# Kernel tuning notes

Hardware: AMD Instinct MI355X
Metric: run time of the kernel (lower is better)

## Reference

```python
import jax, jax.numpy as jnp
import numpy as np

D_MODEL = 1024
NUM_HEADS = 16
HEAD_DIM = D_MODEL // NUM_HEADS  # 64
SCALE = HEAD_DIM ** -0.5
BIAS_LEN = 128  # min(max_seq_len=512, 128)
ROPE_BASE = 10000.0
LN_EPS = 1e-5


def setup_inputs() -> dict:
    key = jax.random.key(0)
    ks = jax.random.split(key, 8)
    B, Lq, Lkv = 8, 512, 512
    return {
        "decoder_hidden": jax.random.normal(ks[0], (B, Lq, D_MODEL), jnp.float32),
        "encoder_output": jax.random.normal(ks[1], (B, Lkv, D_MODEL), jnp.float32),
        "Wqkv": jax.random.normal(ks[2], (3 * D_MODEL, D_MODEL), jnp.float32) * 0.02,
        "Wout": jax.random.normal(ks[3], (D_MODEL, D_MODEL), jnp.float32) * 0.02,
        "b_out": jnp.zeros((D_MODEL,), jnp.float32),
        "Wgate": jax.random.normal(ks[4], (D_MODEL, D_MODEL), jnp.float32) * 0.02,
        "b_gate": jnp.zeros((D_MODEL,), jnp.float32),
        "gamma": jnp.ones((D_MODEL,), jnp.float32),
        "beta": jnp.zeros((D_MODEL,), jnp.float32),
    }


def _layernorm(x, gamma, beta):
    mu = jnp.mean(x, axis=-1, keepdims=True)
    var = jnp.mean(jnp.square(x - mu), axis=-1, keepdims=True)
    return (x - mu) * jax.lax.rsqrt(var + LN_EPS) * gamma + beta


def _rope(x, cos, sin):
    # x: [B, H, L, HEAD_DIM]; cos/sin: [L, HEAD_DIM//2]
    half = HEAD_DIM // 2
    c = cos[None, None, :, :]
    s = sin[None, None, :, :]
    x_even, x_odd = x[..., :half], x[..., half:]
    return jnp.concatenate([x_even * c - x_odd * s, x_even * s + x_odd * c], axis=-1)


def _temporal_bias(L_q, L_kv):
    pos = jnp.arange(BIAS_LEN, dtype=jnp.float32)
    dist = jnp.abs(pos[None, :] - pos[:, None])  # [128,128]
    bias = jnp.exp(-dist * 0.1) - dist * 0.05
    if L_q <= BIAS_LEN and L_kv <= BIAS_LEN:
        return bias[:L_q, :L_kv]
    # bilinear interpolation (align_corners=False / half-pixel) fallback
    return jax.image.resize(bias, (L_q, L_kv), method="bilinear")


def reference(decoder_hidden, encoder_output, Wqkv, Wout, b_out, Wgate, b_gate, gamma, beta):
    B, L_q, _ = decoder_hidden.shape
    L_kv = encoder_output.shape[1]
    residual = decoder_hidden

    q_in = _layernorm(decoder_hidden, gamma, beta)
    kv_in = _layernorm(encoder_output, gamma, beta)

    q = q_in @ Wqkv[:D_MODEL].T
    k = kv_in @ Wqkv[D_MODEL:2 * D_MODEL].T
    v = kv_in @ Wqkv[2 * D_MODEL:].T

    q = q.reshape(B, L_q, NUM_HEADS, HEAD_DIM).transpose(0, 2, 1, 3)
    k = k.reshape(B, L_kv, NUM_HEADS, HEAD_DIM).transpose(0, 2, 1, 3)
    v = v.reshape(B, L_kv, NUM_HEADS, HEAD_DIM).transpose(0, 2, 1, 3)

    # rotary embedding over max(L_q, L_kv) positions
    L = max(L_q, L_kv)
    inv_freq = 1.0 / ROPE_BASE ** (jnp.arange(0, HEAD_DIM, 2, dtype=jnp.float32) / HEAD_DIM)
    freqs = jnp.arange(L, dtype=jnp.float32)[:, None] * inv_freq[None, :]  # [L, HEAD_DIM//2]
    cos, sin = jnp.cos(freqs), jnp.sin(freqs)
    q = _rope(q, cos[:L_q], sin[:L_q])
    k = _rope(k, cos[:L_kv], sin[:L_kv])

    scores = jnp.einsum("bhqd,bhkd->bhqk", q, k) * SCALE
    scores = scores + _temporal_bias(L_q, L_kv)[None, None, :, :]

    attn = jax.nn.softmax(scores, axis=-1)
    attended = jnp.einsum("bhqk,bhkd->bhqd", attn, v)
    attended = attended.transpose(0, 2, 1, 3).reshape(B, L_q, D_MODEL)
    attended = attended @ Wout.T + b_out

    gate = jax.nn.sigmoid(attended @ Wgate.T + b_gate)
    output = gate * attended + (1.0 - gate) * residual
    return output
```

## Files before the change

kernel.cpp:

```cpp
#include <hip/hip_runtime.h>
#include <hip/hip_bf16.h>

#define D_MODEL 1024
#define NHEADS 16
#define HDIM 64
#define BATCH 8
#define SEQ 512
#define NROWS 4096
#define SCALE 0.125f
#define LN_EPS 1e-5f

typedef __attribute__((ext_vector_type(8))) short bf16x8;
typedef __attribute__((ext_vector_type(4))) float f32x4;
typedef __attribute__((ext_vector_type(8))) unsigned short u16x8;

static __device__ __forceinline__ float bf2f(unsigned short u) {
    return __uint_as_float(((unsigned int)u) << 16);
}
static __device__ __forceinline__ unsigned short f2bf(float f) {
    unsigned int x = __float_as_uint(f);
    unsigned int r = (x + 0x7fffu + ((x >> 16) & 1u)) >> 16;
    return (unsigned short)r;
}

#define GLOAD16(gp, lp)                                                        \
    __builtin_amdgcn_global_load_lds(                                          \
        (const __attribute__((address_space(1))) void*)(gp),                   \
        (__attribute__((address_space(3))) void*)(lp), 16, 0, 0)

static __device__ __forceinline__ float bias128(int a, int b) {
    float d = fabsf((float)(a - b));
    return expf(-d * 0.1f) - d * 0.05f;
}

__global__ void prep_kernel(const float* __restrict__ dec, const float* __restrict__ enc,
                            const float* __restrict__ gamma, const float* __restrict__ beta,
                            const float* __restrict__ Wqkv,
                            const float* __restrict__ Wout, const float* __restrict__ Wgate,
                            unsigned short* __restrict__ q_ln, unsigned short* __restrict__ kv_ln,
                            float* __restrict__ bias, unsigned short* __restrict__ Wqkv_bf,
                            unsigned short* __restrict__ Wout_bf, unsigned short* __restrict__ Wgate_bf) {
    int blk = blockIdx.x;
    int t = threadIdx.x;
    if (blk >= 12288) {
        int idx = (blk - 12288) * 256 + t;
        const float* src; unsigned short* dst; int off;
        if (idx < 262144) { src = Wout; dst = Wout_bf; off = idx; }
        else              { src = Wgate; dst = Wgate_bf; off = idx - 262144; }
        float4 v = ((const float4*)src)[off];
        ushort4 u;
        u.x = f2bf(v.x); u.y = f2bf(v.y); u.z = f2bf(v.z); u.w = f2bf(v.w);
        ((ushort4*)dst)[off] = u;
        return;
    }
    if (blk >= 9216) {
        int idx = (blk - 9216) * 256 + t;
        float4 v = ((const float4*)Wqkv)[idx];
        ushort4 u;
        u.x = f2bf(v.x); u.y = f2bf(v.y); u.z = f2bf(v.z); u.w = f2bf(v.w);
        ((ushort4*)Wqkv_bf)[idx] = u;
        return;
    }
    if (blk >= 8192) {
        int idx = (blk - 8192) * 256 + t;
        int qi = idx >> 9, kj = idx & 511;
        float fq = (qi + 0.5f) * 0.25f - 0.5f;
        float fk = (kj + 0.5f) * 0.25f - 0.5f;
        int iq = (int)floorf(fq); float tq = fq - (float)iq;
        int ik = (int)floorf(fk); float tk = fk - (float)ik;
        int iq0 = min(max(iq, 0), 127), iq1 = min(max(iq + 1, 0), 127);
        int ik0 = min(max(ik, 0), 127), ik1 = min(max(ik + 1, 0), 127);
        float v = (1.f - tq) * ((1.f - tk) * bias128(iq0, ik0) + tk * bias128(iq0, ik1))
                +        tq  * ((1.f - tk) * bias128(iq1, ik0) + tk * bias128(iq1, ik1));
        bias[idx] = v;
        return;
    }
    int row = blk;
    const float* src = (row < NROWS) ? dec + (size_t)row * D_MODEL
                                     : enc + (size_t)(row - NROWS) * D_MODEL;
    unsigned short* dst = (row < NROWS) ? q_ln + (size_t)row * D_MODEL
                                        : kv_ln + (size_t)(row - NROWS) * D_MODEL;
    float4 x = ((const float4*)src)[t];
    float s  = x.x + x.y + x.z + x.w;
    float ss = x.x * x.x + x.y * x.y + x.z * x.z + x.w * x.w;
    #pragma unroll
    for (int off = 32; off > 0; off >>= 1) {
        s  += __shfl_down(s, off);
        ss += __shfl_down(ss, off);
    }
    __shared__ float red_s[4], red_ss[4];
    int wid = t >> 6, lane = t & 63;
    if (lane == 0) { red_s[wid] = s; red_ss[wid] = ss; }
    __syncthreads();
    if (t == 0) {
        float S = red_s[0] + red_s[1] + red_s[2] + red_s[3];
        float SS = red_ss[0] + red_ss[1] + red_ss[2] + red_ss[3];
        red_s[0] = S; red_ss[0] = SS;
    }
    __syncthreads();
    float mu  = red_s[0] * (1.0f / 1024.0f);
    float var = red_ss[0] * (1.0f / 1024.0f) - mu * mu;
    float rstd = rsqrtf(var + LN_EPS);
    float4 g = ((const float4*)gamma)[t];
    float4 bb = ((const float4*)beta)[t];
    ushort4 u;
    u.x = f2bf((x.x - mu) * rstd * g.x + bb.x);
    u.y = f2bf((x.y - mu) * rstd * g.y + bb.y);
    u.z = f2bf((x.z - mu) * rstd * g.z + bb.z);
    u.w = f2bf((x.w - mu) * rstd * g.w + bb.w);
    ((ushort4*)dst)[t] = u;
}

__global__ void convert_og(const float* __restrict__ Wout, const float* __restrict__ Wgate,
                           unsigned short* __restrict__ Wout_bf, unsigned short* __restrict__ Wgate_bf) {
    int idx = blockIdx.x * 256 + threadIdx.x;
    const float* src; unsigned short* dst; int off;
    if (idx < 262144) { src = (const float*)Wout; dst = Wout_bf; off = idx; }
    else              { src = (const float*)Wgate; dst = Wgate_bf; off = idx - 262144; }
    float4 v = ((const float4*)src)[off];
    ushort4 u;
    u.x = f2bf(v.x); u.y = f2bf(v.y); u.z = f2bf(v.z); u.w = f2bf(v.w);
    ((ushort4*)dst)[off] = u;
}

#define CSTR 136

struct alignas(16) Smem64B {
    unsigned short A[64 * 128];
    unsigned short B[128 * 128];
};

#define MF(a, b, d) __builtin_amdgcn_mfma_f32_16x16x32_bf16((a), (b), (d), 0, 0, 0)

#define GEMM_KH2B(kh)                                                          \
    {                                                                          \
        int pofs = (((kh) * 4 + quad) ^ c) * 8;                                \
        const unsigned short* Arow_ = &As2[(wr * 32 + c) * 128 + pofs];        \
        const unsigned short* Brow_ = &Bs2[(wc * 64 + c) * 128 + pofs];        \
        bf16x8 f0 = *(const bf16x8*)(Arow_);                                   \
        bf16x8 f1 = *(const bf16x8*)(Arow_ + 2048);                            \
        bf16x8 g0 = *(const bf16x8*)(Brow_);                                   \
        bf16x8 g1 = *(const bf16x8*)(Brow_ + 2048);                            \
        bf16x8 g2 = *(const bf16x8*)(Brow_ + 4096);                            \
        bf16x8 g3 = *(const bf16x8*)(Brow_ + 6144);                            \
        c00 = MF(f0, g0, c00); c01 = MF(f0, g1, c01); c02 = MF(f0, g2, c02); c03 = MF(f0, g3, c03); \
        c10 = MF(f1, g0, c10); c11 = MF(f1, g1, c11); c12 = MF(f1, g2, c12); c13 = MF(f1, g3, c13); \
    }

#define GEMM_BODY_64B(Aptr, Bptr)                                              \
    int wave = tid >> 6, lane = tid & 63, quad = lane >> 4, c = lane & 15;     \
    int wr = wave >> 1, wc = wave & 1;                                         \
    int l4 = lane >> 4, l15 = lane & 15;                                       \
    const unsigned short* Abase = (Aptr) + (size_t)(rt * 64) * 1024;           \
    const unsigned short* Bbase = (Bptr) + (size_t)(ct * 128) * 1024;          \
    int aoff0 = (wave * 16 +  0 + l4) * 1024 + ((l15 ^ ( 0 + l4)) * 8);        \
    int aoff1 = (wave * 16 +  4 + l4) * 1024 + ((l15 ^ ( 4 + l4)) * 8);        \
    int aoff2 = (wave * 16 +  8 + l4) * 1024 + ((l15 ^ ( 8 + l4)) * 8);        \
    int aoff3 = (wave * 16 + 12 + l4) * 1024 + ((l15 ^ (12 + l4)) * 8);        \
    int boff0 = (wave * 32 +  0 + l4) * 1024 + ((l15 ^ (( 0 + l4) & 15)) * 8); \
    int boff1 = (wave * 32 +  4 + l4) * 1024 + ((l15 ^ (( 4 + l4) & 15)) * 8); \
    int boff2 = (wave * 32 +  8 + l4) * 1024 + ((l15 ^ (( 8 + l4) & 15)) * 8); \
    int boff3 = (wave * 32 + 12 + l4) * 1024 + ((l15 ^ ((12 + l4) & 15)) * 8); \
    int boff4 = (wave * 32 + 16 + l4) * 1024 + ((l15 ^ ((16 + l4) & 15)) * 8); \
    int boff5 = (wave * 32 + 20 + l4) * 1024 + ((l15 ^ ((20 + l4) & 15)) * 8); \
    int boff6 = (wave * 32 + 24 + l4) * 1024 + ((l15 ^ ((24 + l4) & 15)) * 8); \
    int boff7 = (wave * 32 + 28 + l4) * 1024 + ((l15 ^ ((28 + l4) & 15)) * 8); \
    unsigned short* AsW = As2 + wave * 2048;                                   \
    unsigned short* BsW = Bs2 + wave * 4096;                                   \
    f32x4 c00 = (f32x4)0.f, c01 = (f32x4)0.f, c02 = (f32x4)0.f, c03 = (f32x4)0.f; \
    f32x4 c10 = (f32x4)0.f, c11 = (f32x4)0.f, c12 = (f32x4)0.f, c13 = (f32x4)0.f; \
    for (int kt = 0; kt < 8; ++kt) {                                           \
        int k0 = kt * 128;                                                     \
        __syncthreads();                                                       \
        GLOAD16(Abase + aoff0 + k0, AsW);                                      \
        GLOAD16(Abase + aoff1 + k0, AsW + 512);                                \
        GLOAD16(Abase + aoff2 + k0, AsW + 1024);                               \
        GLOAD16(Abase + aoff3 + k0, AsW + 1536);                               \
        GLOAD16(Bbase + boff0 + k0, BsW);                                      \
        GLOAD16(Bbase + boff1 + k0, BsW + 512);                                \
        GLOAD16(Bbase + boff2 + k0, BsW + 1024);                               \
        GLOAD16(Bbase + boff3 + k0, BsW + 1536);                               \
        GLOAD16(Bbase + boff4 + k0, BsW + 2048);                               \
        GLOAD16(Bbase + boff5 + k0, BsW + 2560);                               \
        GLOAD16(Bbase + boff6 + k0, BsW + 3072);                               \
        GLOAD16(Bbase + boff7 + k0, BsW + 3584);                               \
        __syncthreads();                                                       \
        GEMM_KH2B(0)                                                           \
        GEMM_KH2B(1)                                                           \
        GEMM_KH2B(2)                                                           \
        GEMM_KH2B(3)                                                           \
    }

union alignas(16) SmemQD {
    struct { unsigned short A[2][64 * 64]; unsigned short B[2][128 * 64]; } ab;
    unsigned short C[64 * CSTR];
    unsigned short Ct[128 * 72];
};

#define QSTAGE(pA, pB, k0)                                                     \
    GLOAD16(Ab + (k0),          (pA) + stW);                                   \
    GLOAD16(Ab + 32768 + (k0),  (pA) + stW + 2048);                            \
    GLOAD16(Bb + (k0),          (pB) + stW);                                   \
    GLOAD16(Bb + 32768 + (k0),  (pB) + stW + 2048);                            \
    GLOAD16(Bb + 65536 + (k0),  (pB) + stW + 4096);                            \
    GLOAD16(Bb + 98304 + (k0),  (pB) + stW + 6144);

#define QKH(pA, pB, kh)                                                        \
    {                                                                          \
        int pofs = (((kh) * 4 + quad) ^ x7) * 8;                               \
        const unsigned short* Ar_ = (pA) + (wr * 32 + c) * 64 + pofs;          \
        const unsigned short* Br_ = (pB) + (wc * 64 + c) * 64 + pofs;          \
        bf16x8 f0 = *(const bf16x8*)(Ar_);                                     \
        bf16x8 f1 = *(const bf16x8*)(Ar_ + 1024);                              \
        bf16x8 g0 = *(const bf16x8*)(Br_);                                     \
        bf16x8 g1 = *(const bf16x8*)(Br_ + 1024);                              \
        bf16x8 g2 = *(const bf16x8*)(Br_ + 2048);                              \
        bf16x8 g3 = *(const bf16x8*)(Br_ + 3072);                              \
        c00 = MF(f0, g0, c00); c01 = MF(f0, g1, c01); c02 = MF(f0, g2, c02); c03 = MF(f0, g3, c03); \
        c10 = MF(f1, g0, c10); c11 = MF(f1, g1, c11); c12 = MF(f1, g2, c12); c13 = MF(f1, g3, c13); \
    }

#define QROPE_REG(i, reg, A0, A1, A2, A3)                                      \
    {                                                                          \
        int mloc = wr * 32 + (i) * 16 + quad * 4 + (reg);                      \
        int crow = mloc * CSTR + wc * 64;                                      \
        float fl = (float)((rt * 64 + mloc) & 511);                            \
        float aa0 = fl * inv0, aa1 = fl * inv1;                                \
        float c0 = cosf(aa0), s0 = sinf(aa0);                                  \
        float c1 = cosf(aa1), s1 = sinf(aa1);                                  \
        float e0 = A0[(reg)], o0 = A2[(reg)];                                  \
        float e1 = A1[(reg)], o1 = A3[(reg)];                                  \
        smemq.C[crow + c]      = f2bf(e0 * c0 - o0 * s0);                      \
        smemq.C[crow + 32 + c] = f2bf(e0 * s0 + o0 * c0);                      \
        smemq.C[crow + 16 + c] = f2bf(e1 * c1 - o1 * s1);                      \
        smemq.C[crow + 48 + c] = f2bf(e1 * s1 + o1 * c1);                      \
    }
#define QROPE_ROW(i, A0, A1, A2, A3)                                           \
    QROPE_REG(i, 0, A0, A1, A2, A3) QROPE_REG(i, 1, A0, A1, A2, A3)            \
    QROPE_REG(i, 2, A0, A1, A2, A3) QROPE_REG(i, 3, A0, A1, A2, A3)

#define QVSECT_REG(i, j, reg, Acc)                                             \
    smemq.Ct[(wc * 64 + (j) * 16 + c) * 72 + (wr * 32 + (i) * 16 + quad * 4 + (reg))] = f2bf(Acc[(reg)]);
#define QVSECT_TILE(i, j, Acc)                                                 \
    QVSECT_REG(i, j, 0, Acc) QVSECT_REG(i, j, 1, Acc)                          \
    QVSECT_REG(i, j, 2, Acc) QVSECT_REG(i, j, 3, Acc)

__global__ __launch_bounds__(256, 1)
void qkv_gemm_mfma(const unsigned short* __restrict__ q_ln,
                   const unsigned short* __restrict__ kv_ln,
                   const unsigned short* __restrict__ Wb,
                   unsigned short* __restrict__ qo,
                   unsigned short* __restrict__ ko,
                   unsigned short* __restrict__ vo) {
    int bid = blockIdx.x;
    int wg = (bid & 7) * 192 + (bid >> 3);
    int st = wg >> 5, in = wg & 31;
    int stc = st >> 4, str = st & 15;
    int ct = stc * 8 + (in & 7);
    int rt = str * 4 + (in >> 3);
    int n0 = ct * 128;
    int section = stc;
    const unsigned short* A = (section == 0) ? q_ln : kv_ln;

    __shared__ SmemQD smemq;
    int tid = threadIdx.x;
    int wave = tid >> 6, lane = tid & 63, quad = lane >> 4, c = lane & 15;
    int wr = wave >> 1, wc = wave & 1;
    int x7 = c & 7;

    int soff = (tid >> 3) * 1024 + (((tid & 7) ^ ((tid >> 3) & 7)) * 8);
    const unsigned short* Ab = A + (size_t)(rt * 64) * 1024 + soff;
    const unsigned short* Bb = Wb + (size_t)n0 * 1024 + soff;
    int stW = wave * 512;
    unsigned short* A0 = smemq.ab.A[0];
    unsigned short* A1 = smemq.ab.A[1];
    unsigned short* B0 = smemq.ab.B[0];
    unsigned short* B1 = smemq.ab.B[1];

    f32x4 c00 = (f32x4)0.f, c01 = (f32x4)0.f, c02 = (f32x4)0.f, c03 = (f32x4)0.f;
    f32x4 c10 = (f32x4)0.f, c11 = (f32x4)0.f, c12 = (f32x4)0.f, c13 = (f32x4)0.f;

    QSTAGE(A0, B0, 0)
    __syncthreads();
    for (int kt2 = 0; kt2 < 8; ++kt2) {
        QSTAGE(A1, B1, (kt2 * 2 + 1) * 64)
        QKH(A0, B0, 0) QKH(A0, B0, 1)
        __syncthreads();
        if (kt2 < 7) { QSTAGE(A0, B0, (kt2 * 2 + 2) * 64) }
        QKH(A1, B1, 0) QKH(A1, B1, 1)
        __syncthreads();
    }

    if (section == 2) {
        QVSECT_TILE(0, 0, c00) QVSECT_TILE(0, 1, c01) QVSECT_TILE(0, 2, c02) QVSECT_TILE(0, 3, c03)
        QVSECT_TILE(1, 0, c10) QVSECT_TILE(1, 1, c11) QVSECT_TILE(1, 2, c12) QVSECT_TILE(1, 3, c13)
        __syncthreads();
        int dr = tid >> 1, hh = tid & 1;
        int h = ((n0 & 1023) >> 6) + (dr >> 6);
        int d = dr & 63;
        int mmb = rt * 64;
        int bb = mmb >> 9, ll0 = mmb & 511;
        unsigned short* orow = vo + (((size_t)bb * NHEADS + h) * HDIM + d) * SEQ + ll0 + hh * 32;
        const unsigned short* csrc = &smemq.Ct[dr * 72 + hh * 32];
        #pragma unroll
        for (int kc = 0; kc < 4; ++kc)
            *(u16x8*)(orow + kc * 8) = *(const u16x8*)(csrc + kc * 8);
        return;
    }

    float inv0 = expf(-0.2878231366f * (float)c);
    float inv1 = expf(-0.2878231366f * (float)(16 + c));
    QROPE_ROW(0, c00, c01, c02, c03)
    QROPE_ROW(1, c10, c11, c12, c13)
    __syncthreads();

    unsigned short* outp = (section == 0) ? qo : ko;
    int rr = tid >> 2;
    int ch = (tid >> 1) & 1;
    int sub = tid & 1;
    int mm = rt * 64 + rr;
    int bb = mm >> 9, ll = mm & 511;
    int h = ((n0 & 1023) >> 6) + ch;
    unsigned short* orow = outp + (((size_t)bb * NHEADS + h) * SEQ + ll) * HDIM + sub * 32;
    const unsigned short* csrc = &smemq.C[rr * CSTR + ch * 64 + sub * 32];
    #pragma unroll
    for (int kc = 0; kc < 4; ++kc)
        *(u16x8*)(orow + kc * 8) = *(const u16x8*)(csrc + kc * 8);
}

#define O1_REG(mb, reg, n, Acc)                                                \
    t_bf[(size_t)((mb) + (reg)) * 1024 + (n)] = f2bf(Acc[(reg)] + bo);
#define O1_TILE(i, j, Acc)                                                     \
    {                                                                          \
        int n = ct * 128 + wc * 64 + (j) * 16 + c;                             \
        float bo = b_out[n];                                                   \
        int mb = rt * 64 + wr * 32 + (i) * 16 + quad * 4;                      \
        O1_REG(mb, 0, n, Acc) O1_REG(mb, 1, n, Acc)                            \
        O1_REG(mb, 2, n, Acc) O1_REG(mb, 3, n, Acc)                            \
    }

__global__ __launch_bounds__(256, 1)
void out_gemm1_mfma(const unsigned short* __restrict__ att,
                    const unsigned short* __restrict__ Wob,
                    const float* __restrict__ b_out,
                    unsigned short* __restrict__ t_bf) {
    int ct = blockIdx.x, rt = blockIdx.y;
    __shared__ Smem64B smem2;
    unsigned short* As2 = smem2.A;
    unsigned short* Bs2 = smem2.B;
    int tid = threadIdx.x;

    GEMM_BODY_64B(att, Wob)

    O1_TILE(0, 0, c00) O1_TILE(0, 1, c01) O1_TILE(0, 2, c02) O1_TILE(0, 3, c03)
    O1_TILE(1, 0, c10) O1_TILE(1, 1, c11) O1_TILE(1, 2, c12) O1_TILE(1, 3, c13)
}

#define O2_REG(mb, reg, n, Acc)                                                \
    {                                                                          \
        float gz = Acc[(reg)] + bg;                                            \
        float g = 1.0f / (1.0f + expf(-gz));                                   \
        size_t idx = (size_t)((mb) + (reg)) * 1024 + (n);                      \
        float tv = bf2f(t_bf[idx]);                                            \
        float rv = residual[idx];                                              \
        out[idx] = g * tv + (1.0f - g) * rv;                                   \
    }
#define O2_TILE(i, j, Acc)                                                     \
    {                                                                          \
        int n = ct * 128 + wc * 64 + (j) * 16 + c;                             \
        float bg = b_gate[n];                                                  \
        int mb = rt * 64 + wr * 32 + (i) * 16 + quad * 4;                      \
        O2_REG(mb, 0, n, Acc) O2_REG(mb, 1, n, Acc)                            \
        O2_REG(mb, 2, n, Acc) O2_REG(mb, 3, n, Acc)                            \
    }

__global__ __launch_bounds__(256, 1)
void out_gemm2_mfma(const unsigned short* __restrict__ t_bf,
                    const unsigned short* __restrict__ Wgb,
                    const float* __restrict__ b_gate,
                    const float* __restrict__ residual,
                    float* __restrict__ out) {
    int ct = blockIdx.x, rt = blockIdx.y;
    __shared__ Smem64B smem2;
    unsigned short* As2 = smem2.A;
    unsigned short* Bs2 = smem2.B;
    int tid = threadIdx.x;

    GEMM_BODY_64B(t_bf, Wgb)

    O2_TILE(0, 0, c00) O2_TILE(0, 1, c01) O2_TILE(0, 2, c02) O2_TILE(0, 3, c03)
    O2_TILE(1, 0, c10) O2_TILE(1, 1, c11) O2_TILE(1, 2, c12) O2_TILE(1, 3, c13)
}

#define KSTR 72

__global__ __launch_bounds__(512)
void attn_kernel(const unsigned short* __restrict__ q,
                 const unsigned short* __restrict__ k,
                 const unsigned short* __restrict__ vt,
                 const float* __restrict__ bias,
                 unsigned short* __restrict__ attended) {
    int qt = blockIdx.x, h = blockIdx.y, b = blockIdx.z;
    __shared__ unsigned short Ks[64 * 64];
    __shared__ unsigned short Vs[64 * 64];
    __shared__ unsigned short Ps[128 * KSTR];
    __shared__ float lf[128];

    int tid = threadIdx.x;
    int wave = tid >> 6, lane = tid & 63;
    int quad = lane >> 4, c = lane & 15;
    int wb = wave * 16;
    size_t headbase = (((size_t)b * NHEADS + h) * SEQ) * HDIM;
    int q0 = qt * 128;

    const unsigned short* qrow = q + headbase + (size_t)(q0 + wb + c) * HDIM;
    bf16x8 aq0 = *(const bf16x8*)(qrow + quad * 8);
    bf16x8 aq1 = *(const bf16x8*)(qrow + 32 + quad * 8);

    int srow = wave * 8 + (lane >> 3);
    int schunk = (lane & 7) ^ (srow & 7);
    unsigned short* KsW = Ks + wave * 512;
    unsigned short* VsW = Vs + wave * 512;
    const unsigned short* kgb = k + headbase + (size_t)srow * HDIM + schunk * 8;
    const unsigned short* vgb = vt + headbase + (size_t)srow * SEQ + schunk * 8;
    int x7 = c & 7;
    int p0 = (quad ^ x7) * 8;
    int p1 = ((4 + quad) ^ x7) * 8;

    f32x4 oacc[4];
    #pragma unroll
    for (int t = 0; t < 4; ++t) oacc[t] = (f32x4)0.f;
    float lrow[4];
    #pragma unroll
    for (int r = 0; r < 4; ++r) lrow[r] = 0.f;

    for (int kt = 0; kt < 8; ++kt) {
        int kv0 = kt * 64;
        __syncthreads();
        GLOAD16(kgb + (size_t)kv0 * HDIM, KsW);
        GLOAD16(vgb + kv0, VsW);
        __syncthreads();

        f32x4 sacc[4];
        #pragma unroll
        for (int nt = 0; nt < 4; ++nt) {
            const unsigned short* kbase = &Ks[(nt * 16 + c) * 64];
            bf16x8 b0 = *(const bf16x8*)(kbase + p0);
            bf16x8 b1 = *(const bf16x8*)(kbase + p1);
            f32x4 a = (f32x4)0.f;
            a = __builtin_amdgcn_mfma_f32_16x16x32_bf16(aq0, b0, a, 0, 0, 0);
            a = __builtin_amdgcn_mfma_f32_16x16x32_bf16(aq1, b1, a, 0, 0, 0);
            sacc[nt] = a;
        }

        const float* bbase = bias + (size_t)(q0 + wb + quad * 4) * 512 + kv0 + c;
        float tsum[4];
        #pragma unroll
        for (int r = 0; r < 4; ++r) tsum[r] = 0.f;
        #pragma unroll
        for (int nt = 0; nt < 4; ++nt)
            #pragma unroll
            for (int r = 0; r < 4; ++r) {
                float p = __expf(sacc[nt][r] * SCALE + bbase[(size_t)r * 512 + nt * 16]);
                tsum[r] += p;
                Ps[(wb + quad * 4 + r) * KSTR + nt * 16 + c] = f2bf(p);
            }
        #pragma unroll
        for (int r = 0; r < 4; ++r) {
            float t = tsum[r];
            t += __shfl_xor(t, 1);
            t += __shfl_xor(t, 2);
            t += __shfl_xor(t, 4);
            t += __shfl_xor(t, 8);
            lrow[r] += t;
        }

        bf16x8 pb0 = *(const bf16x8*)&Ps[(wb + c) * KSTR + quad * 8];
        bf16x8 pb1 = *(const bf16x8*)&Ps[(wb + c) * KSTR + 32 + quad * 8];
        #pragma unroll
        for (int t = 0; t < 4; ++t) {
            const unsigned short* vbase = &Vs[(t * 16 + c) * 64];
            bf16x8 a0 = *(const bf16x8*)(vbase + p0);
            bf16x8 a1 = *(const bf16x8*)(vbase + p1);
            oacc[t] = __builtin_amdgcn_mfma_f32_16x16x32_bf16(a0, pb0, oacc[t], 0, 0, 0);
            oacc[t] = __builtin_amdgcn_mfma_f32_16x16x32_bf16(a1, pb1, oacc[t], 0, 0, 0);
        }
    }

    if (c == 0) {
        f32x4 lv;
        lv[0] = lrow[0]; lv[1] = lrow[1]; lv[2] = lrow[2]; lv[3] = lrow[3];
        *(f32x4*)&lf[wb + quad * 4] = lv;
    }
    float invl = 1.0f / lf[wb + c];
    unsigned short* drow = attended + ((size_t)b * SEQ + (q0 + wb + c)) * D_MODEL + h * HDIM;
    #pragma unroll
    for (int t = 0; t < 4; ++t) {
        ushort4 o;
        o.x = f2bf(oacc[t][0] * invl);
        o.y = f2bf(oacc[t][1] * invl);
        o.z = f2bf(oacc[t][2] * invl);
        o.w = f2bf(oacc[t][3] * invl);
        *(ushort4*)(drow + t * 16 + quad * 4) = o;
    }
}

extern "C" void kernel_launch(void* const* d_in, const int* in_sizes, int n_in,
                              void* d_out, int out_size, void* d_ws, size_t ws_size,
                              hipStream_t stream) {
    const float* dec    = (const float*)d_in[0];
    const float* enc    = (const float*)d_in[1];
    const float* Wqkv   = (const float*)d_in[2];
    const float* Wout   = (const float*)d_in[3];
    const float* b_out  = (const float*)d_in[4];
    const float* Wgate  = (const float*)d_in[5];
    const float* b_gate = (const float*)d_in[6];
    const float* gamma  = (const float*)d_in[7];
    const float* beta   = (const float*)d_in[8];
    float* out = (float*)d_out;

    char* ws = (char*)d_ws;
    const size_t MB = 1024 * 1024;
    unsigned short* q_ln    = (unsigned short*)(ws + 0 * MB);
    unsigned short* kv_ln   = (unsigned short*)(ws + 8 * MB);
    unsigned short* qb      = (unsigned short*)(ws + 16 * MB);
    unsigned short* kb      = (unsigned short*)(ws + 24 * MB);
    unsigned short* vb      = (unsigned short*)(ws + 32 * MB);
    unsigned short* Wqkv_bf = (unsigned short*)(ws + 40 * MB);
    float*          bias    = (float*)(ws + 46 * MB);
    unsigned short* att     = (unsigned short*)(ws + 0 * MB);
    unsigned short* t_bf    = (unsigned short*)(ws + 24 * MB);

    bool hoist = (ws_size >= 51 * MB);
    unsigned short* Wout_bf  = (unsigned short*)(ws + (hoist ? 47 * MB : 32 * MB));
    unsigned short* Wgate_bf = (unsigned short*)(ws + (hoist ? 49 * MB : 34 * MB));

    prep_kernel<<<hoist ? 14336 : 12288, 256, 0, stream>>>(
        dec, enc, gamma, beta, Wqkv, Wout, Wgate,
        q_ln, kv_ln, bias, Wqkv_bf, Wout_bf, Wgate_bf);
    qkv_gemm_mfma<<<1536, 256, 0, stream>>>(q_ln, kv_ln, Wqkv_bf, qb, kb, vb);
    attn_kernel<<<dim3(4, 16, 8), 512, 0, stream>>>(qb, kb, vb, bias, att);
    if (!hoist)
        convert_og<<<2048, 256, 0, stream>>>(Wout, Wgate, Wout_bf, Wgate_bf);
    out_gemm1_mfma<<<dim3(8, 64), 256, 0, stream>>>(att, Wout_bf, b_out, t_bf);
    out_gemm2_mfma<<<dim3(8, 64), 256, 0, stream>>>(t_bf, Wgate_bf, b_gate, dec, out);
}
```

Baseline: 208.9 us.

## Double-buffer K/V tiles in attention and deepen QKV GEMM prefetch with vmcnt waits

The attention kernel now keeps two K/V shared-memory buffers and prefetches the next tile while the current one is computed. Explicit s_waitcnt vmcnt plus raw s_barrier replace the __syncthreads calls. The QKV GEMM gets the same treatment, issuing two stages ahead and waiting on partial vmcnt. This aims to hide global-to-LDS load latency. It costs more LDS per block and relies on correct hand-counted vmcnt values, including the wait that covers the bias global loads inside the step.

```diff
diff --git a/kernel.cpp b/kernel.cpp
--- a/kernel.cpp
+++ b/kernel.cpp
@@ -27,6 +27,9 @@
     __builtin_amdgcn_global_load_lds(                                          \
         (const __attribute__((address_space(1))) void*)(gp),                   \
         (__attribute__((address_space(3))) void*)(lp), 16, 0, 0)
+
+#define VMW(n) asm volatile("s_waitcnt vmcnt(" #n ")" ::: "memory")
+#define RBAR() __builtin_amdgcn_s_barrier()
 
 static __device__ __forceinline__ float bias128(int a, int b) {
     float d = fabsf((float)(a - b));
@@ -281,14 +284,18 @@
     f32x4 c10 = (f32x4)0.f, c11 = (f32x4)0.f, c12 = (f32x4)0.f, c13 = (f32x4)0.f;
 
     QSTAGE(A0, B0, 0)
-    __syncthreads();
+    QSTAGE(A1, B1, 64)
+    VMW(6); RBAR();
     for (int kt2 = 0; kt2 < 8; ++kt2) {
-        QSTAGE(A1, B1, (kt2 * 2 + 1) * 64)
         QKH(A0, B0, 0) QKH(A0, B0, 1)
-        __syncthreads();
-        if (kt2 < 7) { QSTAGE(A0, B0, (kt2 * 2 + 2) * 64) }
+        RBAR();
+        if (kt2 < 7) { QSTAGE(A0, B0, (kt2 * 2 + 2) * 64) VMW(6); }
+        else         { VMW(0); }
+        RBAR();
         QKH(A1, B1, 0) QKH(A1, B1, 1)
-        __syncthreads();
+        RBAR();
+        if (kt2 < 7) { QSTAGE(A1, B1, (kt2 * 2 + 3) * 64) VMW(6); }
+        RBAR();
     }
 
     if (section == 2) {
@@ -394,6 +401,60 @@
 
 #define KSTR 72
 
+static __device__ __forceinline__ void attn_step(
+    const unsigned short* __restrict__ KsB, const unsigned short* __restrict__ VsB,
+    int kv0, const float* __restrict__ bias, unsigned short* __restrict__ Ps,
+    int q0, int wb, int quad, int c, int p0, int p1,
+    bf16x8 aq0, bf16x8 aq1, f32x4 (&oacc)[4], float (&lrow)[4])
+{
+    f32x4 sacc[4];
+    #pragma unroll
+    for (int nt = 0; nt < 4; ++nt) {
+        const unsigned short* kbase = &KsB[(nt * 16 + c) * 64];
+        bf16x8 b0 = *(const bf16x8*)(kbase + p0);
+        bf16x8 b1 = *(const bf16x8*)(kbase + p1);
+        f32x4 a = (f32x4)0.f;
+        a = __builtin_amdgcn_mfma_f32_16x16x32_bf16(aq0, b0, a, 0, 0, 0);
+        a = __builtin_amdgcn_mfma_f32_16x16x32_bf16(aq1, b1, a, 0, 0, 0);
+        sacc[nt] = a;
+    }
+    const float* bbase = bias + (size_t)(q0 + wb + quad * 4) * 512 + kv0 + c;
+    float tsum[4];
+    #pragma unroll
+    for (int r = 0; r < 4; ++r) tsum[r] = 0.f;
+    #pragma unroll
+    for (int nt = 0; nt < 4; ++nt)
+        #pragma unroll
+        for (int r = 0; r < 4; ++r) {
+            float p = __expf(sacc[nt][r] * SCALE + bbase[(size_t)r * 512 + nt * 16]);
+            tsum[r] += p;
+            Ps[(wb + quad * 4 + r) * KSTR + nt * 16 + c] = f2bf(p);
+        }
+    #pragma unroll
+    for (int r = 0; r < 4; ++r) {
+        float t = tsum[r];
+        t += __shfl_xor(t, 1);
+        t += __shfl_xor(t, 2);
+        t += __shfl_xor(t, 4);
+        t += __shfl_xor(t, 8);
+        lrow[r] += t;
+    }
+    bf16x8 pb0 = *(const bf16x8*)&Ps[(wb + c) * KSTR + quad * 8];
+    bf16x8 pb1 = *(const bf16x8*)&Ps[(wb + c) * KSTR + 32 + quad * 8];
+    #pragma unroll
+    for (int t = 0; t < 4; ++t) {
+        const unsigned short* vbase = &VsB[(t * 16 + c) * 64];
+        bf16x8 a0 = *(const bf16x8*)(vbase + p0);
+        bf16x8 a1 = *(const bf16x8*)(vbase + p1);
+        oacc[t] = __builtin_amdgcn_mfma_f32_16x16x32_bf16(a0, pb0, oacc[t], 0, 0, 0);
+        oacc[t] = __builtin_amdgcn_mfma_f32_16x16x32_bf16(a1, pb1, oacc[t], 0, 0, 0);
+    }
+}
+
+#define ASTAGE(BUF, kvt)                                                       \
+    GLOAD16(kgb + (size_t)((kvt) * 64) * HDIM, Ks[BUF] + wave * 512);          \
+    GLOAD16(vgb + (kvt) * 64, Vs[BUF] + wave * 512);
+
 __global__ __launch_bounds__(512)
 void attn_kernel(const unsigned short* __restrict__ q,
                  const unsigned short* __restrict__ k,
@@ -401,8 +462,8 @@
                  const float* __restrict__ bias,
                  unsigned short* __restrict__ attended) {
     int qt = blockIdx.x, h = blockIdx.y, b = blockIdx.z;
-    __shared__ unsigned short Ks[64 * 64];
-    __shared__ unsigned short Vs[64 * 64];
+    __shared__ unsigned short Ks[2][64 * 64];
+    __shared__ unsigned short Vs[2][64 * 64];
     __shared__ unsigned short Ps[128 * KSTR];
     __shared__ float lf[128];
 
@@ -419,8 +480,6 @@
 
     int srow = wave * 8 + (lane >> 3);
     int schunk = (lane & 7) ^ (srow & 7);
-    unsigned short* KsW = Ks + wave * 512;
-    unsigned short* VsW = Vs + wave * 512;
     const unsigned short* kgb = k + headbase + (size_t)srow * HDIM + schunk * 8;
     const unsigned short* vgb = vt + headbase + (size_t)srow * SEQ + schunk * 8;
     int x7 = c & 7;
@@ -434,57 +493,21 @@
     #pragma unroll
     for (int r = 0; r < 4; ++r) lrow[r] = 0.f;
 
-    for (int kt = 0; kt < 8; ++kt) {
-        int kv0 = kt * 64;
-        __syncthreads();
-        GLOAD16(kgb + (size_t)kv0 * HDIM, KsW);
-        GLOAD16(vgb + kv0, VsW);
-        __syncthreads();
-
-        f32x4 sacc[4];
-        #pragma unroll
-        for (int nt = 0; nt < 4; ++nt) {
-            const unsigned short* kbase = &Ks[(nt * 16 + c) * 64];
-            bf16x8 b0 = *(const bf16x8*)(kbase + p0);
-            bf16x8 b1 = *(const bf16x8*)(kbase + p1);
-            f32x4 a = (f32x4)0.f;
-            a = __builtin_amdgcn_mfma_f32_16x16x32_bf16(aq0, b0, a, 0, 0, 0);
-            a = __builtin_amdgcn_mfma_f32_16x16x32_bf16(aq1, b1, a, 0, 0, 0);
-            sacc[nt] = a;
-        }
-
-        const float* bbase = bias + (size_t)(q0 + wb + quad * 4) * 512 + kv0 + c;
-        float tsum[4];
-        #pragma unroll
-        for (int r = 0; r < 4; ++r) tsum[r] = 0.f;
-        #pragma unroll
-        for (int nt = 0; nt < 4; ++nt)
-            #pragma unroll
-            for (int r = 0; r < 4; ++r) {
-                float p = __expf(sacc[nt][r] * SCALE + bbase[(size_t)r * 512 + nt * 16]);
-                tsum[r] += p;
-                Ps[(wb + quad * 4 + r) * KSTR + nt * 16 + c] = f2bf(p);
-            }
-        #pragma unroll
-        for (int r = 0; r < 4; ++r) {
-            float t = tsum[r];
-            t += __shfl_xor(t, 1);
-            t += __shfl_xor(t, 2);
-            t += __shfl_xor(t, 4);
-            t += __shfl_xor(t, 8);
-            lrow[r] += t;
-        }
-
-        bf16x8 pb0 = *(const bf16x8*)&Ps[(wb + c) * KSTR + quad * 8];
-        bf16x8 pb1 = *(const bf16x8*)&Ps[(wb + c) * KSTR + 32 + quad * 8];
-        #pragma unroll
-        for (int t = 0; t < 4; ++t) {
-            const unsigned short* vbase = &Vs[(t * 16 + c) * 64];
-            bf16x8 a0 = *(const bf16x8*)(vbase + p0);
-            bf16x8 a1 = *(const bf16x8*)(vbase + p1);
-            oacc[t] = __builtin_amdgcn_mfma_f32_16x16x32_bf16(a0, pb0, oacc[t], 0, 0, 0);
-            oacc[t] = __builtin_amdgcn_mfma_f32_16x16x32_bf16(a1, pb1, oacc[t], 0, 0, 0);
-        }
+    ASTAGE(0, 0)
+    ASTAGE(1, 1)
+    VMW(2); RBAR();
+    for (int kt2 = 0; kt2 < 4; ++kt2) {
+        attn_step(Ks[0], Vs[0], (kt2 * 2) * 64, bias, Ps,
+                  q0, wb, quad, c, p0, p1, aq0, aq1, oacc, lrow);
+        RBAR();
+        if (kt2 < 3) { ASTAGE(0, kt2 * 2 + 2) VMW(2); }
+        else         { VMW(0); }
+        RBAR();
+        attn_step(Ks[1], Vs[1], (kt2 * 2 + 1) * 64, bias, Ps,
+                  q0, wb, quad, c, p0, p1, aq0, aq1, oacc, lrow);
+        RBAR();
+        if (kt2 < 3) { ASTAGE(1, kt2 * 2 + 3) VMW(2); }
+        RBAR();
     }
 
     if (c == 0) {
```

Result: no change. 208.3 us (-0.3%).
